# Performance work log

Hardware: AMD Instinct MI355X
Metric: run time of the kernel (lower is better)

The kernel has to match this reference:

```python
import jax, jax.numpy as jnp
from jax import lax
import numpy as np

B, L, D = 16, 512, 256
F, K = 256, 3
M = 2048
EPS = 1e-5


def setup_inputs() -> dict:
    key = jax.random.key(0)
    ks = jax.random.split(key, 12)
    x = jax.random.normal(ks[0], (B, L, D), jnp.float32)
    # integer durations >= 1, sum over L <= 3*512 = 1536 < M, as in training targets
    target = jax.random.randint(ks[1], (B, L), 1, 4)
    s = 0.02
    conv1_w = jax.random.normal(ks[2], (F, D, K), jnp.float32) * s
    conv1_b = jnp.zeros((F,), jnp.float32)
    ln1_g = jnp.ones((F,), jnp.float32)
    ln1_b = jnp.zeros((F,), jnp.float32)
    conv2_w = jax.random.normal(ks[3], (F, F, K), jnp.float32) * s
    conv2_b = jnp.zeros((F,), jnp.float32)
    ln2_g = jnp.ones((F,), jnp.float32)
    ln2_b = jnp.zeros((F,), jnp.float32)
    lin_w = jax.random.normal(ks[4], (F, 1), jnp.float32) * s
    lin_b = jnp.zeros((1,), jnp.float32)
    return dict(x=x, target=target, mel_max_length=M,
                conv1_w=conv1_w, conv1_b=conv1_b, ln1_g=ln1_g, ln1_b=ln1_b,
                conv2_w=conv2_w, conv2_b=conv2_b, ln2_g=ln2_g, ln2_b=ln2_b,
                lin_w=lin_w, lin_b=lin_b)


def _layer_norm(h, g, b):
    mu = jnp.mean(h, axis=-1, keepdims=True)
    var = jnp.mean(jnp.square(h - mu), axis=-1, keepdims=True)
    return (h - mu) * lax.rsqrt(var + EPS) * g + b


def _conv1d(h_bld, w, b):
    # h: (B, L, C_in), w: (C_out, C_in, K) -> (B, L, C_out), SAME padding
    pad = (w.shape[-1] - 1) // 2
    h = jnp.transpose(h_bld, (0, 2, 1))  # (B, C, L)
    h = lax.conv_general_dilated(h, w, (1,), [(pad, pad)],
                                 dimension_numbers=('NCH', 'OIH', 'NCH'))
    return jnp.transpose(h + b[None, :, None], (0, 2, 1))


def _duration_predictor(x, conv1_w, conv1_b, ln1_g, ln1_b,
                        conv2_w, conv2_b, ln2_g, ln2_b, lin_w, lin_b):
    # FastSpeech duration predictor (eval mode: dropout = identity)
    h = jax.nn.relu(_layer_norm(_conv1d(x, conv1_w, conv1_b), ln1_g, ln1_b))
    h = jax.nn.relu(_layer_norm(_conv1d(h, conv2_w, conv2_b), ln2_g, ln2_b))
    return jax.nn.relu(h @ lin_w + lin_b)[..., 0]  # (B, L)


def _length_regulate(x, dur, mel_max_length):
    # alignment[b,m,l] = 1 iff cs[l-1] <= m < cs[l]  (exactly the scatter+diff trick
    # of create_alignment, padded to mel_max_length as in the original F.pad)
    cs = jnp.cumsum(dur, axis=1)              # (B, L) inclusive cumsum
    prev = cs - dur                           # exclusive cumsum
    m = jnp.arange(mel_max_length)[None, :, None]  # (1, M, 1)
    align = ((m >= prev[:, None, :]) & (m < cs[:, None, :])).astype(x.dtype)  # (B,M,L)
    return jnp.einsum('bml,bld->bmd', align, x)


def reference(x, target, mel_max_length, conv1_w, conv1_b, ln1_g, ln1_b,
              conv2_w, conv2_b, ln2_g, ln2_b, lin_w, lin_b):
    dup = _duration_predictor(x, conv1_w, conv1_b, ln1_g, ln1_b,
                              conv2_w, conv2_b, ln2_g, ln2_b, lin_w, lin_b)
    output = _length_regulate(x, target, mel_max_length)
    return (output, dup)
```

## Files before the change

kernel.cpp:

```cpp
#include <hip/hip_runtime.h>
#include <hip/hip_bf16.h>

#define Bn 16
#define Ln 512
#define Cn 256
#define Fn 256
#define Kn 3
#define Mn 2048

#define NKSTEP 24
#define MT 32
#define XS_PS 264
#define NCONVBLK 256

typedef __attribute__((ext_vector_type(8))) short short8;
typedef __attribute__((ext_vector_type(4))) float f32x4;

static __device__ __forceinline__ unsigned short f2bf(float f) {
    unsigned int u = __float_as_uint(f);
    return (unsigned short)((u + 0x7fff + ((u >> 16) & 1)) >> 16);
}

__global__ __launch_bounds__(256) void pack_scan(
    const float* __restrict__ w1, const float* __restrict__ w2,
    unsigned short* __restrict__ bp1, unsigned short* __restrict__ bp2,
    const int* __restrict__ target, int* __restrict__ map)
{
    __shared__ int ss[256];
    const int blk = blockIdx.x;
    const int t = threadIdx.x;
    if (blk < 1536) {
        int i = blk * 256 + t;
        const float* w = w1;
        unsigned short* bp = bp1;
        if (i >= Fn * Cn * Kn) { i -= Fn * Cn * Kn; w = w2; bp = bp2; }
        int j    = i & 7;
        int lane = (i >> 3) & 63;
        int nt   = (i >> 9) & 15;
        int s    = i >> 13;
        int kap = s * 32 + ((lane >> 4) * 8) + j;
        int k = kap >> 8;
        int d = kap & 255;
        int f = nt * 16 + (lane & 15);
        bp[i] = f2bf(w[(f * Cn + d) * Kn + k]);
    } else {
        int b = blk - 1536;
        int v0 = target[b * Ln + 2 * t];
        int v1 = target[b * Ln + 2 * t + 1];
        ss[t] = v0 + v1;
        __syncthreads();
        for (int off = 1; off < 256; off <<= 1) {
            int add = (t >= off) ? ss[t - off] : 0;
            __syncthreads();
            ss[t] += add;
            __syncthreads();
        }
        int S     = ss[t];
        int total = ss[255];
        int cs1   = S;
        int cs0   = S - v1;
        int prev0 = cs0 - v0;
        for (int m = prev0; m < cs0; ++m) map[b * Mn + m] = 2 * t;
        for (int m = cs0;   m < cs1; ++m) map[b * Mn + m] = 2 * t + 1;
        for (int m = total + t; m < Mn; m += 256) map[b * Mn + m] = -1;
    }
}

template <bool IS_F32_IN, bool DO_LINEAR, bool WITH_REG>
__global__ __launch_bounds__(256) void conv_mfma(
    const void* __restrict__ in_,
    const unsigned short* __restrict__ bp,
    const float* __restrict__ bias,
    const float* __restrict__ gamma,
    const float* __restrict__ beta,
    const float* __restrict__ lw,
    const float* __restrict__ lb,
    unsigned short* __restrict__ hout,
    float* __restrict__ dup,
    const float* __restrict__ gx,
    const int* __restrict__ gmap,
    float* __restrict__ gout)
{
    __shared__ __align__(16) unsigned short xs[(MT + 2) * XS_PS];
    __shared__ float2 red[MT][4];
    __shared__ float  red2[MT][4];

    const int t = threadIdx.x;

    if (WITH_REG && blockIdx.x >= NCONVBLK) {
        int e4 = (blockIdx.x - NCONVBLK) * 256 + t;
        int d4 = e4 & 63;
        int bm = e4 >> 6;
        int b  = bm >> 11;
        int l  = gmap[bm];
        float4 val = make_float4(0.f, 0.f, 0.f, 0.f);
        if (l >= 0) val = *((const float4*)(gx + (size_t)(b * Ln + l) * Cn) + d4);
        ((float4*)gout)[e4] = val;
        return;
    }

    const int b  = blockIdx.x >> 4;
    const int l0 = (blockIdx.x & 15) * MT;

    if (IS_F32_IN) {
        const float* in = (const float*)in_;
        for (int idx = t; idx < (MT + 2) * 64; idx += 256) {
            int row = idx >> 6;
            int c4  = (idx & 63) * 4;
            int l = l0 + row - 1;
            float4 v = make_float4(0.f, 0.f, 0.f, 0.f);
            if (l >= 0 && l < Ln) v = *(const float4*)&in[((size_t)b * Ln + l) * Cn + c4];
            unsigned int lo = (unsigned int)f2bf(v.x) | ((unsigned int)f2bf(v.y) << 16);
            unsigned int hi = (unsigned int)f2bf(v.z) | ((unsigned int)f2bf(v.w) << 16);
            *(uint2*)&xs[row * XS_PS + c4] = make_uint2(lo, hi);
        }
    } else {
        const unsigned short* in = (const unsigned short*)in_;
        for (int idx = t; idx < (MT + 2) * 32; idx += 256) {
            int row = idx >> 5;
            int c8  = (idx & 31) * 8;
            int l = l0 + row - 1;
            uint4 v = make_uint4(0u, 0u, 0u, 0u);
            if (l >= 0 && l < Ln) v = *(const uint4*)&in[((size_t)b * Ln + l) * Cn + c8];
            *(uint4*)&xs[row * XS_PS + c8] = v;
        }
    }
    __syncthreads();

    const int lane = t & 63;
    const int wv   = t >> 6;
    const int mrow = lane & 15;
    const int q    = lane >> 4;

    f32x4  acc[2][4] = {};
    short8 bfr[2][4];
    short8 afr[2][2];

    auto loadB = [&](int s, int slot) {
        const unsigned short* p = bp + (size_t)((s * 16 + wv * 4) * 64 + lane) * 8;
        #pragma unroll
        for (int i = 0; i < 4; ++i)
            bfr[slot][i] = *(const short8*)(p + (size_t)i * 64 * 8);
    };
    auto loadA = [&](int s, int slot) {
        const int k    = s >> 3;
        const int dcol = (s & 7) * 32 + q * 8;
        #pragma unroll
        for (int mt = 0; mt < 2; ++mt)
            afr[slot][mt] = *(const short8*)&xs[(mt * 16 + mrow + k) * XS_PS + dcol];
    };

    loadB(0, 0); loadA(0, 0);
    loadB(1, 1); loadA(1, 1);

    #pragma unroll 2
    for (int s = 0; s < NKSTEP; ++s) {
        const int slot = s & 1;
        #pragma unroll
        for (int mt = 0; mt < 2; ++mt)
            #pragma unroll
            for (int i = 0; i < 4; ++i)
                acc[mt][i] = __builtin_amdgcn_mfma_f32_16x16x32_bf16(
                    afr[slot][mt], bfr[slot][i], acc[mt][i], 0, 0, 0);
        const int sn = (s + 2 < NKSTEP) ? (s + 2) : s;
        loadB(sn, slot);
        loadA(sn, slot);
    }

    float gv[4], bv[4], lwv[4], biasv[4];
    #pragma unroll
    for (int i = 0; i < 4; ++i) {
        int col = wv * 64 + i * 16 + mrow;
        biasv[i] = bias[col];
        gv[i]    = gamma[col];
        bv[i]    = beta[col];
        if (DO_LINEAR) lwv[i] = lw[col];
    }
    #pragma unroll
    for (int mt = 0; mt < 2; ++mt)
        #pragma unroll
        for (int i = 0; i < 4; ++i)
            #pragma unroll
            for (int r = 0; r < 4; ++r)
                acc[mt][i][r] += biasv[i];

    #pragma unroll
    for (int mt = 0; mt < 2; ++mt)
        #pragma unroll
        for (int r = 0; r < 4; ++r) {
            float s  = acc[mt][0][r] + acc[mt][1][r] + acc[mt][2][r] + acc[mt][3][r];
            float sq = acc[mt][0][r] * acc[mt][0][r] + acc[mt][1][r] * acc[mt][1][r]
                     + acc[mt][2][r] * acc[mt][2][r] + acc[mt][3][r] * acc[mt][3][r];
            #pragma unroll
            for (int off = 1; off <= 8; off <<= 1) {
                s  += __shfl_xor(s,  off, 64);
                sq += __shfl_xor(sq, off, 64);
            }
            if (mrow == 0) red[mt * 16 + q * 4 + r][wv] = make_float2(s, sq);
        }
    __syncthreads();

    float muv[2][4], rsv[2][4];
    #pragma unroll
    for (int mt = 0; mt < 2; ++mt)
        #pragma unroll
        for (int r = 0; r < 4; ++r) {
            int row = mt * 16 + q * 4 + r;
            float2 p0 = red[row][0], p1 = red[row][1], p2 = red[row][2], p3 = red[row][3];
            float s  = p0.x + p1.x + p2.x + p3.x;
            float sq = p0.y + p1.y + p2.y + p3.y;
            float mu  = s * (1.f / 256.f);
            float var = sq * (1.f / 256.f) - mu * mu;
            muv[mt][r] = mu;
            rsv[mt][r] = rsqrtf(var + 1e-5f);
        }

    if (!DO_LINEAR) {
        #pragma unroll
        for (int mt = 0; mt < 2; ++mt)
            #pragma unroll
            for (int r = 0; r < 4; ++r) {
                int l = l0 + mt * 16 + q * 4 + r;
                size_t base = ((size_t)b * Ln + l) * Fn;
                #pragma unroll
                for (int i = 0; i < 4; ++i) {
                    float o = fmaxf((acc[mt][i][r] - muv[mt][r]) * rsv[mt][r] * gv[i] + bv[i], 0.f);
                    hout[base + wv * 64 + i * 16 + mrow] = f2bf(o);
                }
            }
    } else {
        #pragma unroll
        for (int mt = 0; mt < 2; ++mt)
            #pragma unroll
            for (int r = 0; r < 4; ++r) {
                float dot = 0.f;
                #pragma unroll
                for (int i = 0; i < 4; ++i) {
                    float o = fmaxf((acc[mt][i][r] - muv[mt][r]) * rsv[mt][r] * gv[i] + bv[i], 0.f);
                    dot += o * lwv[i];
                }
                #pragma unroll
                for (int off = 1; off <= 8; off <<= 1)
                    dot += __shfl_xor(dot, off, 64);
                if (mrow == 0) red2[mt * 16 + q * 4 + r][wv] = dot;
            }
        __syncthreads();
        if (t < MT) {
            float d = red2[t][0] + red2[t][1] + red2[t][2] + red2[t][3];
            dup[b * Ln + l0 + t] = fmaxf(d + lb[0], 0.f);
        }
    }
}

extern "C" void kernel_launch(void* const* d_in, const int* in_sizes, int n_in,
                              void* d_out, int out_size, void* d_ws, size_t ws_size,
                              hipStream_t stream) {
    const float* x    = (const float*)d_in[0];
    const int*   targ = (const int*)d_in[1];
    const float* c1w = (const float*)d_in[3];
    const float* c1b = (const float*)d_in[4];
    const float* g1  = (const float*)d_in[5];
    const float* be1 = (const float*)d_in[6];
    const float* c2w = (const float*)d_in[7];
    const float* c2b = (const float*)d_in[8];
    const float* g2  = (const float*)d_in[9];
    const float* be2 = (const float*)d_in[10];
    const float* lw  = (const float*)d_in[11];
    const float* lb  = (const float*)d_in[12];

    float* out     = (float*)d_out;
    float* out_dup = out + (size_t)Bn * Mn * Cn;

    char* ws = (char*)d_ws;
    unsigned short* bp1 = (unsigned short*)ws;
    unsigned short* bp2 = (unsigned short*)(ws + 393216);
    unsigned short* h1  = (unsigned short*)(ws + 2 * 393216);
    int*            map = (int*)(ws + 2 * 393216 + 4194304);

    pack_scan<<<1552, 256, 0, stream>>>(c1w, c2w, bp1, bp2, targ, map);

    conv_mfma<true, false, true><<<NCONVBLK + (Bn * Mn * Cn / 4) / 256, 256, 0, stream>>>(
        (const void*)x, bp1, c1b, g1, be1, nullptr, nullptr, h1, nullptr,
        x, map, out);

    conv_mfma<false, true, false><<<NCONVBLK, 256, 0, stream>>>(
        (const void*)h1, bp2, c2b, g2, be2, lw, lb, nullptr, out_dup,
        nullptr, nullptr, nullptr);
}
```

Baseline: 116.6 us.

## Fuse pack, scan, both convs and gather into one cooperative kernel

```diff
diff --git a/kernel.cpp b/kernel.cpp
--- a/kernel.cpp
+++ b/kernel.cpp
@@ -1,5 +1,8 @@
 #include <hip/hip_runtime.h>
 #include <hip/hip_bf16.h>
+#include <hip/hip_cooperative_groups.h>
+
+namespace cg = cooperative_groups;
 
 #define Bn 16
 #define Ln 512
@@ -11,7 +14,6 @@
 #define NKSTEP 24
 #define MT 32
 #define XS_PS 264
-#define NCONVBLK 256
 
 typedef __attribute__((ext_vector_type(8))) short short8;
 typedef __attribute__((ext_vector_type(4))) float f32x4;
@@ -21,53 +23,21 @@
     return (unsigned short)((u + 0x7fff + ((u >> 16) & 1)) >> 16);
 }
 
-__global__ __launch_bounds__(256) void pack_scan(
-    const float* __restrict__ w1, const float* __restrict__ w2,
-    unsigned short* __restrict__ bp1, unsigned short* __restrict__ bp2,
-    const int* __restrict__ target, int* __restrict__ map)
+static __device__ __forceinline__ void gather_one(
+    const float* __restrict__ gx, const int* __restrict__ gmap,
+    float* __restrict__ gout, int e4)
 {
-    __shared__ int ss[256];
-    const int blk = blockIdx.x;
-    const int t = threadIdx.x;
-    if (blk < 1536) {
-        int i = blk * 256 + t;
-        const float* w = w1;
-        unsigned short* bp = bp1;
-        if (i >= Fn * Cn * Kn) { i -= Fn * Cn * Kn; w = w2; bp = bp2; }
-        int j    = i & 7;
-        int lane = (i >> 3) & 63;
-        int nt   = (i >> 9) & 15;
-        int s    = i >> 13;
-        int kap = s * 32 + ((lane >> 4) * 8) + j;
-        int k = kap >> 8;
-        int d = kap & 255;
-        int f = nt * 16 + (lane & 15);
-        bp[i] = f2bf(w[(f * Cn + d) * Kn + k]);
-    } else {
-        int b = blk - 1536;
-        int v0 = target[b * Ln + 2 * t];
-        int v1 = target[b * Ln + 2 * t + 1];
-        ss[t] = v0 + v1;
-        __syncthreads();
-        for (int off = 1; off < 256; off <<= 1) {
-            int add = (t >= off) ? ss[t - off] : 0;
-            __syncthreads();
-            ss[t] += add;
-            __syncthreads();
-        }
-        int S     = ss[t];
-        int total = ss[255];
-        int cs1   = S;
-        int cs0   = S - v1;
-        int prev0 = cs0 - v0;
-        for (int m = prev0; m < cs0; ++m) map[b * Mn + m] = 2 * t;
-        for (int m = cs0;   m < cs1; ++m) map[b * Mn + m] = 2 * t + 1;
-        for (int m = total + t; m < Mn; m += 256) map[b * Mn + m] = -1;
-    }
-}
-
-template <bool IS_F32_IN, bool DO_LINEAR, bool WITH_REG>
-__global__ __launch_bounds__(256) void conv_mfma(
+    int d4 = e4 & 63;
+    int bm = e4 >> 6;
+    int b  = bm >> 11;
+    int l  = gmap[bm];
+    float4 val = make_float4(0.f, 0.f, 0.f, 0.f);
+    if (l >= 0) val = *((const float4*)(gx + (size_t)(b * Ln + l) * Cn) + d4);
+    ((float4*)gout)[e4] = val;
+}
+
+template <bool IS_F32_IN, bool DO_LINEAR>
+static __device__ __forceinline__ void conv_phase(
     const void* __restrict__ in_,
     const unsigned short* __restrict__ bp,
     const float* __restrict__ bias,
@@ -77,30 +47,11 @@
     const float* __restrict__ lb,
     unsigned short* __restrict__ hout,
     float* __restrict__ dup,
-    const float* __restrict__ gx,
-    const int* __restrict__ gmap,
-    float* __restrict__ gout)
+    int cblk, int t,
+    unsigned short* xs, float2 (*red)[4], float (*red2)[4])
 {
-    __shared__ __align__(16) unsigned short xs[(MT + 2) * XS_PS];
-    __shared__ float2 red[MT][4];
-    __shared__ float  red2[MT][4];
-
-    const int t = threadIdx.x;
-
-    if (WITH_REG && blockIdx.x >= NCONVBLK) {
-        int e4 = (blockIdx.x - NCONVBLK) * 256 + t;
-        int d4 = e4 & 63;
-        int bm = e4 >> 6;
-        int b  = bm >> 11;
-        int l  = gmap[bm];
-        float4 val = make_float4(0.f, 0.f, 0.f, 0.f);
-        if (l >= 0) val = *((const float4*)(gx + (size_t)(b * Ln + l) * Cn) + d4);
-        ((float4*)gout)[e4] = val;
-        return;
-    }
-
-    const int b  = blockIdx.x >> 4;
-    const int l0 = (blockIdx.x & 15) * MT;
+    const int b  = cblk >> 4;
+    const int l0 = (cblk & 15) * MT;
 
     if (IS_F32_IN) {
         const float* in = (const float*)in_;
@@ -252,6 +203,78 @@
     }
 }
 
+__global__ __launch_bounds__(256) void fused(
+    const float* __restrict__ x, const int* __restrict__ target,
+    const float* __restrict__ c1w, const float* __restrict__ c1b,
+    const float* __restrict__ g1,  const float* __restrict__ be1,
+    const float* __restrict__ c2w, const float* __restrict__ c2b,
+    const float* __restrict__ g2,  const float* __restrict__ be2,
+    const float* __restrict__ lw,  const float* __restrict__ lb,
+    unsigned short* __restrict__ bp1, unsigned short* __restrict__ bp2,
+    unsigned short* __restrict__ h1,  int* __restrict__ map,
+    float* __restrict__ out, float* __restrict__ out_dup)
+{
+    __shared__ __align__(16) unsigned short xs[(MT + 2) * XS_PS];
+    __shared__ float2 red[MT][4];
+    __shared__ float  red2[MT][4];
+    __shared__ int    ss[256];
+
+    const int blk = blockIdx.x;
+    const int t   = threadIdx.x;
+    cg::grid_group grid = cg::this_grid();
+
+    if (blk < 16) {
+        const int bb = blk;
+        int v0 = target[bb * Ln + 2 * t];
+        int v1 = target[bb * Ln + 2 * t + 1];
+        ss[t] = v0 + v1;
+        __syncthreads();
+        for (int off = 1; off < 256; off <<= 1) {
+            int add = (t >= off) ? ss[t - off] : 0;
+            __syncthreads();
+            ss[t] += add;
+            __syncthreads();
+        }
+        int S     = ss[t];
+        int total = ss[255];
+        int cs1   = S;
+        int cs0   = S - v1;
+        int prev0 = cs0 - v0;
+        for (int m = prev0; m < cs0; ++m) map[bb * Mn + m] = 2 * t;
+        for (int m = cs0;   m < cs1; ++m) map[bb * Mn + m] = 2 * t + 1;
+        for (int m = total + t; m < Mn; m += 256) map[bb * Mn + m] = -1;
+    } else if (blk < 208) {
+        int v = (blk - 16) * 256 + t;
+        const float* w = c1w;
+        unsigned short* bp = bp1;
+        if (v >= 24576) { v -= 24576; w = c2w; bp = bp2; }
+        int lane = v & 63, nt = (v >> 6) & 15, s = v >> 10;
+        int f    = nt * 16 + (lane & 15);
+        int kap0 = s * 32 + (lane >> 4) * 8;
+        const float* p = w + ((size_t)f * Cn + (kap0 & 255)) * Kn + (kap0 >> 8);
+        short8 o;
+        #pragma unroll
+        for (int j = 0; j < 8; ++j) o[j] = (short)f2bf(p[3 * j]);
+        *(short8*)(bp + (size_t)v * 8) = o;
+    }
+
+    grid.sync();
+
+    conv_phase<true, false>(x, bp1, c1b, g1, be1, nullptr, nullptr, h1, nullptr,
+                            blk, t, xs, red, red2);
+    {
+        const int base = blk * 256 + t;
+        #pragma unroll 4
+        for (int i = 0; i < 32; ++i)
+            gather_one(x, map, out, base + i * 65536);
+    }
+
+    grid.sync();
+
+    conv_phase<false, true>(h1, bp2, c2b, g2, be2, lw, lb, nullptr, out_dup,
+                            blk, t, xs, red, red2);
+}
+
 extern "C" void kernel_launch(void* const* d_in, const int* in_sizes, int n_in,
                               void* d_out, int out_size, void* d_ws, size_t ws_size,
                               hipStream_t stream) {
@@ -277,13 +300,14 @@
     unsigned short* h1  = (unsigned short*)(ws + 2 * 393216);
     int*            map = (int*)(ws + 2 * 393216 + 4194304);
 
-    pack_scan<<<1552, 256, 0, stream>>>(c1w, c2w, bp1, bp2, targ, map);
-
-    conv_mfma<true, false, true><<<NCONVBLK + (Bn * Mn * Cn / 4) / 256, 256, 0, stream>>>(
-        (const void*)x, bp1, c1b, g1, be1, nullptr, nullptr, h1, nullptr,
-        x, map, out);
-
-    conv_mfma<false, true, false><<<NCONVBLK, 256, 0, stream>>>(
-        (const void*)h1, bp2, c2b, g2, be2, lw, lb, nullptr, out_dup,
-        nullptr, nullptr, nullptr);
-}
+    void* args[] = {
+        (void*)&x, (void*)&targ,
+        (void*)&c1w, (void*)&c1b, (void*)&g1, (void*)&be1,
+        (void*)&c2w, (void*)&c2b, (void*)&g2, (void*)&be2,
+        (void*)&lw, (void*)&lb,
+        (void*)&bp1, (void*)&bp2, (void*)&h1, (void*)&map,
+        (void*)&out, (void*)&out_dup
+    };
+    hipLaunchCooperativeKernel((const void*)fused, dim3(256), dim3(256),
+                               args, 0, stream);
+}
```

Measured after the change: 203.3 us. 1.74x slower.

## Fuse both conv layers into one kernel with halo recompute of layer one

Applied to the files above, without the earlier changes.

```diff
diff --git a/kernel.cpp b/kernel.cpp
--- a/kernel.cpp
+++ b/kernel.cpp
@@ -11,6 +11,9 @@
 #define NKSTEP 24
 #define MT 32
 #define XS_PS 264
+#define XROWS 50
+#define HROWS 48
+#define HOFF  8
 #define NCONVBLK 256
 
 typedef __attribute__((ext_vector_type(8))) short short8;
@@ -29,24 +32,10 @@
     __shared__ int ss[256];
     const int blk = blockIdx.x;
     const int t = threadIdx.x;
-    if (blk < 1536) {
-        int i = blk * 256 + t;
-        const float* w = w1;
-        unsigned short* bp = bp1;
-        if (i >= Fn * Cn * Kn) { i -= Fn * Cn * Kn; w = w2; bp = bp2; }
-        int j    = i & 7;
-        int lane = (i >> 3) & 63;
-        int nt   = (i >> 9) & 15;
-        int s    = i >> 13;
-        int kap = s * 32 + ((lane >> 4) * 8) + j;
-        int k = kap >> 8;
-        int d = kap & 255;
-        int f = nt * 16 + (lane & 15);
-        bp[i] = f2bf(w[(f * Cn + d) * Kn + k]);
-    } else {
-        int b = blk - 1536;
-        int v0 = target[b * Ln + 2 * t];
-        int v1 = target[b * Ln + 2 * t + 1];
+    if (blk < 16) {
+        const int bb = blk;
+        int v0 = target[bb * Ln + 2 * t];
+        int v1 = target[bb * Ln + 2 * t + 1];
         ss[t] = v0 + v1;
         __syncthreads();
         for (int off = 1; off < 256; off <<= 1) {
@@ -60,70 +49,66 @@
         int cs1   = S;
         int cs0   = S - v1;
         int prev0 = cs0 - v0;
-        for (int m = prev0; m < cs0; ++m) map[b * Mn + m] = 2 * t;
-        for (int m = cs0;   m < cs1; ++m) map[b * Mn + m] = 2 * t + 1;
-        for (int m = total + t; m < Mn; m += 256) map[b * Mn + m] = -1;
+        for (int m = prev0; m < cs0; ++m) map[bb * Mn + m] = 2 * t;
+        for (int m = cs0;   m < cs1; ++m) map[bb * Mn + m] = 2 * t + 1;
+        for (int m = total + t; m < Mn; m += 256) map[bb * Mn + m] = -1;
+    } else {
+        int v = (blk - 16) * 256 + t;
+        const float* w = w1;
+        unsigned short* bp = bp1;
+        if (v >= 24576) { v -= 24576; w = w2; bp = bp2; }
+        int lane = v & 63, nt = (v >> 6) & 15, s = v >> 10;
+        int f    = nt * 16 + (lane & 15);
+        int kap0 = s * 32 + (lane >> 4) * 8;
+        const float* p = w + ((size_t)f * Cn + (kap0 & 255)) * Kn + (kap0 >> 8);
+        short8 o;
+        #pragma unroll
+        for (int j = 0; j < 8; ++j) o[j] = (short)f2bf(p[3 * j]);
+        *(short8*)(bp + (size_t)v * 8) = o;
     }
 }
 
-template <bool IS_F32_IN, bool DO_LINEAR, bool WITH_REG>
-__global__ __launch_bounds__(256) void conv_mfma(
-    const void* __restrict__ in_,
-    const unsigned short* __restrict__ bp,
-    const float* __restrict__ bias,
-    const float* __restrict__ gamma,
-    const float* __restrict__ beta,
-    const float* __restrict__ lw,
-    const float* __restrict__ lb,
-    unsigned short* __restrict__ hout,
-    float* __restrict__ dup,
-    const float* __restrict__ gx,
+__global__ __launch_bounds__(256, 4) void conv12_gather(
+    const float* __restrict__ x,
+    const unsigned short* __restrict__ bp1,
+    const unsigned short* __restrict__ bp2,
+    const float* __restrict__ c1b, const float* __restrict__ g1, const float* __restrict__ be1,
+    const float* __restrict__ c2b, const float* __restrict__ g2, const float* __restrict__ be2,
+    const float* __restrict__ lw,  const float* __restrict__ lb,
     const int* __restrict__ gmap,
-    float* __restrict__ gout)
+    float* __restrict__ out,
+    float* __restrict__ dup)
 {
-    __shared__ __align__(16) unsigned short xs[(MT + 2) * XS_PS];
-    __shared__ float2 red[MT][4];
+    __shared__ __align__(16) unsigned short xs[XROWS * XS_PS];
+    __shared__ float2 red[HROWS][4];
     __shared__ float  red2[MT][4];
 
     const int t = threadIdx.x;
 
-    if (WITH_REG && blockIdx.x >= NCONVBLK) {
+    if (blockIdx.x >= NCONVBLK) {
         int e4 = (blockIdx.x - NCONVBLK) * 256 + t;
         int d4 = e4 & 63;
         int bm = e4 >> 6;
         int b  = bm >> 11;
         int l  = gmap[bm];
         float4 val = make_float4(0.f, 0.f, 0.f, 0.f);
-        if (l >= 0) val = *((const float4*)(gx + (size_t)(b * Ln + l) * Cn) + d4);
-        ((float4*)gout)[e4] = val;
+        if (l >= 0) val = *((const float4*)(x + (size_t)(b * Ln + l) * Cn) + d4);
+        ((float4*)out)[e4] = val;
         return;
     }
 
     const int b  = blockIdx.x >> 4;
     const int l0 = (blockIdx.x & 15) * MT;
 
-    if (IS_F32_IN) {
-        const float* in = (const float*)in_;
-        for (int idx = t; idx < (MT + 2) * 64; idx += 256) {
-            int row = idx >> 6;
-            int c4  = (idx & 63) * 4;
-            int l = l0 + row - 1;
-            float4 v = make_float4(0.f, 0.f, 0.f, 0.f);
-            if (l >= 0 && l < Ln) v = *(const float4*)&in[((size_t)b * Ln + l) * Cn + c4];
-            unsigned int lo = (unsigned int)f2bf(v.x) | ((unsigned int)f2bf(v.y) << 16);
-            unsigned int hi = (unsigned int)f2bf(v.z) | ((unsigned int)f2bf(v.w) << 16);
-            *(uint2*)&xs[row * XS_PS + c4] = make_uint2(lo, hi);
-        }
-    } else {
-        const unsigned short* in = (const unsigned short*)in_;
-        for (int idx = t; idx < (MT + 2) * 32; idx += 256) {
-            int row = idx >> 5;
-            int c8  = (idx & 31) * 8;
-            int l = l0 + row - 1;
-            uint4 v = make_uint4(0u, 0u, 0u, 0u);
-            if (l >= 0 && l < Ln) v = *(const uint4*)&in[((size_t)b * Ln + l) * Cn + c8];
-            *(uint4*)&xs[row * XS_PS + c8] = v;
-        }
+    for (int idx = t; idx < XROWS * 64; idx += 256) {
+        int row = idx >> 6;
+        int c4  = (idx & 63) * 4;
+        int l = l0 - 9 + row;
+        float4 v = make_float4(0.f, 0.f, 0.f, 0.f);
+        if (l >= 0 && l < Ln) v = *(const float4*)&x[((size_t)b * Ln + l) * Cn + c4];
+        unsigned int lo = (unsigned int)f2bf(v.x) | ((unsigned int)f2bf(v.y) << 16);
+        unsigned int hi = (unsigned int)f2bf(v.z) | ((unsigned int)f2bf(v.w) << 16);
+        *(uint2*)&xs[row * XS_PS + c4] = make_uint2(lo, hi);
     }
     __syncthreads();
 
@@ -132,111 +117,197 @@
     const int mrow = lane & 15;
     const int q    = lane >> 4;
 
-    f32x4  acc[2][4] = {};
+    f32x4  acc1[3][4] = {};
     short8 bfr[2][4];
-    short8 afr[2][2];
-
-    auto loadB = [&](int s, int slot) {
-        const unsigned short* p = bp + (size_t)((s * 16 + wv * 4) * 64 + lane) * 8;
+    short8 afr[2][3];
+
+    auto loadB1 = [&](int s, int slot) {
+        const unsigned short* p = bp1 + (size_t)((s * 16 + wv * 4) * 64 + lane) * 8;
         #pragma unroll
         for (int i = 0; i < 4; ++i)
             bfr[slot][i] = *(const short8*)(p + (size_t)i * 64 * 8);
     };
-    auto loadA = [&](int s, int slot) {
+    auto loadA1 = [&](int s, int slot) {
         const int k    = s >> 3;
         const int dcol = (s & 7) * 32 + q * 8;
         #pragma unroll
-        for (int mt = 0; mt < 2; ++mt)
+        for (int mt = 0; mt < 3; ++mt)
             afr[slot][mt] = *(const short8*)&xs[(mt * 16 + mrow + k) * XS_PS + dcol];
     };
 
-    loadB(0, 0); loadA(0, 0);
-    loadB(1, 1); loadA(1, 1);
+    loadB1(0, 0); loadA1(0, 0);
+    loadB1(1, 1); loadA1(1, 1);
 
     #pragma unroll 2
     for (int s = 0; s < NKSTEP; ++s) {
         const int slot = s & 1;
         #pragma unroll
-        for (int mt = 0; mt < 2; ++mt)
+        for (int mt = 0; mt < 3; ++mt)
             #pragma unroll
             for (int i = 0; i < 4; ++i)
-                acc[mt][i] = __builtin_amdgcn_mfma_f32_16x16x32_bf16(
-                    afr[slot][mt], bfr[slot][i], acc[mt][i], 0, 0, 0);
+                acc1[mt][i] = __builtin_amdgcn_mfma_f32_16x16x32_bf16(
+                    afr[slot][mt], bfr[slot][i], acc1[mt][i], 0, 0, 0);
         const int sn = (s + 2 < NKSTEP) ? (s + 2) : s;
-        loadB(sn, slot);
-        loadA(sn, slot);
-    }
-
-    float gv[4], bv[4], lwv[4], biasv[4];
-    #pragma unroll
-    for (int i = 0; i < 4; ++i) {
-        int col = wv * 64 + i * 16 + mrow;
-        biasv[i] = bias[col];
-        gv[i]    = gamma[col];
-        bv[i]    = beta[col];
-        if (DO_LINEAR) lwv[i] = lw[col];
-    }
-    #pragma unroll
-    for (int mt = 0; mt < 2; ++mt)
+        loadB1(sn, slot);
+        loadA1(sn, slot);
+    }
+
+    {
+        float gv[4], bv[4], biasv[4];
+        #pragma unroll
+        for (int i = 0; i < 4; ++i) {
+            int col = wv * 64 + i * 16 + mrow;
+            biasv[i] = c1b[col];
+            gv[i]    = g1[col];
+            bv[i]    = be1[col];
+        }
+        #pragma unroll
+        for (int mt = 0; mt < 3; ++mt)
+            #pragma unroll
+            for (int i = 0; i < 4; ++i)
+                #pragma unroll
+                for (int r = 0; r < 4; ++r)
+                    acc1[mt][i][r] += biasv[i];
+
+        #pragma unroll
+        for (int mt = 0; mt < 3; ++mt)
+            #pragma unroll
+            for (int r = 0; r < 4; ++r) {
+                float s  = acc1[mt][0][r] + acc1[mt][1][r] + acc1[mt][2][r] + acc1[mt][3][r];
+                float sq = acc1[mt][0][r] * acc1[mt][0][r] + acc1[mt][1][r] * acc1[mt][1][r]
+                         + acc1[mt][2][r] * acc1[mt][2][r] + acc1[mt][3][r] * acc1[mt][3][r];
+                #pragma unroll
+                for (int off = 1; off <= 8; off <<= 1) {
+                    s  += __shfl_xor(s,  off, 64);
+                    sq += __shfl_xor(sq, off, 64);
+                }
+                if (mrow == 0) red[mt * 16 + q * 4 + r][wv] = make_float2(s, sq);
+            }
+        __syncthreads();
+
+        float muv[3][4], rsv[3][4];
+        #pragma unroll
+        for (int mt = 0; mt < 3; ++mt)
+            #pragma unroll
+            for (int r = 0; r < 4; ++r) {
+                int row = mt * 16 + q * 4 + r;
+                float2 p0 = red[row][0], p1 = red[row][1], p2 = red[row][2], p3 = red[row][3];
+                float s  = p0.x + p1.x + p2.x + p3.x;
+                float sq = p0.y + p1.y + p2.y + p3.y;
+                float mu  = s * (1.f / 256.f);
+                float var = sq * (1.f / 256.f) - mu * mu;
+                muv[mt][r] = mu;
+                rsv[mt][r] = rsqrtf(var + 1e-5f);
+            }
+
+        #pragma unroll
+        for (int mt = 0; mt < 3; ++mt)
+            #pragma unroll
+            for (int r = 0; r < 4; ++r) {
+                int jr = mt * 16 + q * 4 + r;
+                int l  = l0 - HOFF + jr;
+                bool ok = (l >= 0 && l < Ln);
+                #pragma unroll
+                for (int i = 0; i < 4; ++i) {
+                    float o = ok ? fmaxf((acc1[mt][i][r] - muv[mt][r]) * rsv[mt][r] * gv[i] + bv[i], 0.f)
+                                 : 0.f;
+                    xs[jr * XS_PS + (wv * 64 + i * 16 + mrow)] = f2bf(o);
+                }
+            }
+    }
+    __syncthreads();
+
+    f32x4  acc2[2][4] = {};
+    short8 afr2[2][2];
+
+    auto loadB2 = [&](int s, int slot) {
+        const unsigned short* p = bp2 + (size_t)((s * 16 + wv * 4) * 64 + lane) * 8;
         #pragma unroll
         for (int i = 0; i < 4; ++i)
-            #pragma unroll
-            for (int r = 0; r < 4; ++r)
-                acc[mt][i][r] += biasv[i];
-
-    #pragma unroll
-    for (int mt = 0; mt < 2; ++mt)
-        #pragma unroll
-        for (int r = 0; r < 4; ++r) {
-            float s  = acc[mt][0][r] + acc[mt][1][r] + acc[mt][2][r] + acc[mt][3][r];
-            float sq = acc[mt][0][r] * acc[mt][0][r] + acc[mt][1][r] * acc[mt][1][r]
-                     + acc[mt][2][r] * acc[mt][2][r] + acc[mt][3][r] * acc[mt][3][r];
-            #pragma unroll
-            for (int off = 1; off <= 8; off <<= 1) {
-                s  += __shfl_xor(s,  off, 64);
-                sq += __shfl_xor(sq, off, 64);
-            }
-            if (mrow == 0) red[mt * 16 + q * 4 + r][wv] = make_float2(s, sq);
+            bfr[slot][i] = *(const short8*)(p + (size_t)i * 64 * 8);
+    };
+    auto loadA2 = [&](int s, int slot) {
+        const int k    = s >> 3;
+        const int dcol = (s & 7) * 32 + q * 8;
+        #pragma unroll
+        for (int mt = 0; mt < 2; ++mt)
+            afr2[slot][mt] = *(const short8*)&xs[(mt * 16 + mrow + k + 7) * XS_PS + dcol];
+    };
+
+    loadB2(0, 0); loadA2(0, 0);
+    loadB2(1, 1); loadA2(1, 1);
+
+    #pragma unroll 2
+    for (int s = 0; s < NKSTEP; ++s) {
+        const int slot = s & 1;
+        #pragma unroll
+        for (int mt = 0; mt < 2; ++mt)
+            #pragma unroll
+            for (int i = 0; i < 4; ++i)
+                acc2[mt][i] = __builtin_amdgcn_mfma_f32_16x16x32_bf16(
+                    afr2[slot][mt], bfr[slot][i], acc2[mt][i], 0, 0, 0);
+        const int sn = (s + 2 < NKSTEP) ? (s + 2) : s;
+        loadB2(sn, slot);
+        loadA2(sn, slot);
+    }
+
+    {
+        float gv[4], bv[4], biasv[4], lwv[4];
+        #pragma unroll
+        for (int i = 0; i < 4; ++i) {
+            int col = wv * 64 + i * 16 + mrow;
+            biasv[i] = c2b[col];
+            gv[i]    = g2[col];
+            bv[i]    = be2[col];
+            lwv[i]   = lw[col];
         }
-    __syncthreads();
-
-    float muv[2][4], rsv[2][4];
-    #pragma unroll
-    for (int mt = 0; mt < 2; ++mt)
-        #pragma unroll
-        for (int r = 0; r < 4; ++r) {
-            int row = mt * 16 + q * 4 + r;
-            float2 p0 = red[row][0], p1 = red[row][1], p2 = red[row][2], p3 = red[row][3];
-            float s  = p0.x + p1.x + p2.x + p3.x;
-            float sq = p0.y + p1.y + p2.y + p3.y;
-            float mu  = s * (1.f / 256.f);
-            float var = sq * (1.f / 256.f) - mu * mu;
-            muv[mt][r] = mu;
-            rsv[mt][r] = rsqrtf(var + 1e-5f);
-        }
-
-    if (!DO_LINEAR) {
-        #pragma unroll
-        for (int mt = 0; mt < 2; ++mt)
-            #pragma unroll
-            for (int r = 0; r < 4; ++r) {
-                int l = l0 + mt * 16 + q * 4 + r;
-                size_t base = ((size_t)b * Ln + l) * Fn;
+        #pragma unroll
+        for (int mt = 0; mt < 2; ++mt)
+            #pragma unroll
+            for (int i = 0; i < 4; ++i)
+                #pragma unroll
+                for (int r = 0; r < 4; ++r)
+                    acc2[mt][i][r] += biasv[i];
+
+        #pragma unroll
+        for (int mt = 0; mt < 2; ++mt)
+            #pragma unroll
+            for (int r = 0; r < 4; ++r) {
+                float s  = acc2[mt][0][r] + acc2[mt][1][r] + acc2[mt][2][r] + acc2[mt][3][r];
+                float sq = acc2[mt][0][r] * acc2[mt][0][r] + acc2[mt][1][r] * acc2[mt][1][r]
+                         + acc2[mt][2][r] * acc2[mt][2][r] + acc2[mt][3][r] * acc2[mt][3][r];
+                #pragma unroll
+                for (int off = 1; off <= 8; off <<= 1) {
+                    s  += __shfl_xor(s,  off, 64);
+                    sq += __shfl_xor(sq, off, 64);
+                }
+                if (mrow == 0) red[mt * 16 + q * 4 + r][wv] = make_float2(s, sq);
+            }
+        __syncthreads();
+
+        float muv[2][4], rsv[2][4];
+        #pragma unroll
+        for (int mt = 0; mt < 2; ++mt)
+            #pragma unroll
+            for (int r = 0; r < 4; ++r) {
+                int row = mt * 16 + q * 4 + r;
+                float2 p0 = red[row][0], p1 = red[row][1], p2 = red[row][2], p3 = red[row][3];
+                float s  = p0.x + p1.x + p2.x + p3.x;
+                float sq = p0.y + p1.y + p2.y + p3.y;
+                float mu  = s * (1.f / 256.f);
+                float var = sq * (1.f / 256.f) - mu * mu;
+                muv[mt][r] = mu;
+                rsv[mt][r] = rsqrtf(var + 1e-5f);
+            }
+
+        #pragma unroll
+        for (int mt = 0; mt < 2; ++mt)
+            #pragma unroll
+            for (int r = 0; r < 4; ++r) {
+                float dot = 0.f;
                 #pragma unroll
                 for (int i = 0; i < 4; ++i) {
-                    float o = fmaxf((acc[mt][i][r] - muv[mt][r]) * rsv[mt][r] * gv[i] + bv[i], 0.f);
-                    hout[base + wv * 64 + i * 16 + mrow] = f2bf(o);
-                }
-            }
-    } else {
-        #pragma unroll
-        for (int mt = 0; mt < 2; ++mt)
-            #pragma unroll
-            for (int r = 0; r < 4; ++r) {
-                float dot = 0.f;
-                #pragma unroll
-                for (int i = 0; i < 4; ++i) {
-                    float o = fmaxf((acc[mt][i][r] - muv[mt][r]) * rsv[mt][r] * gv[i] + bv[i], 0.f);
+                    float o = fmaxf((acc2[mt][i][r] - muv[mt][r]) * rsv[mt][r] * gv[i] + bv[i], 0.f);
                     dot += o * lwv[i];
                 }
                 #pragma unroll
@@ -274,16 +345,11 @@
     char* ws = (char*)d_ws;
     unsigned short* bp1 = (unsigned short*)ws;
     unsigned short* bp2 = (unsigned short*)(ws + 393216);
-    unsigned short* h1  = (unsigned short*)(ws + 2 * 393216);
-    int*            map = (int*)(ws + 2 * 393216 + 4194304);
-
-    pack_scan<<<1552, 256, 0, stream>>>(c1w, c2w, bp1, bp2, targ, map);
-
-    conv_mfma<true, false, true><<<NCONVBLK + (Bn * Mn * Cn / 4) / 256, 256, 0, stream>>>(
-        (const void*)x, bp1, c1b, g1, be1, nullptr, nullptr, h1, nullptr,
-        x, map, out);
-
-    conv_mfma<false, true, false><<<NCONVBLK, 256, 0, stream>>>(
-        (const void*)h1, bp2, c2b, g2, be2, lw, lb, nullptr, out_dup,
-        nullptr, nullptr, nullptr);
+    int*            map = (int*)(ws + 2 * 393216);
+
+    pack_scan<<<208, 256, 0, stream>>>(c1w, c2w, bp1, bp2, targ, map);
+
+    conv12_gather<<<NCONVBLK + (Bn * Mn * Cn / 4) / 256, 256, 0, stream>>>(
+        x, bp1, bp2, c1b, g1, be1, c2b, g2, be2, lw, lb,
+        map, out, out_dup);
 }
```

Result: slower. 132.7 us (+13.8%).

## Split length-regulate gather across both conv kernels and vectorize weight packing

Applied to the files above, without the earlier changes.

```diff
diff --git a/kernel.cpp b/kernel.cpp
--- a/kernel.cpp
+++ b/kernel.cpp
@@ -12,6 +12,7 @@
 #define MT 32
 #define XS_PS 264
 #define NCONVBLK 256
+#define NGHALF 1024
 
 typedef __attribute__((ext_vector_type(8))) short short8;
 typedef __attribute__((ext_vector_type(4))) float f32x4;
@@ -29,24 +30,10 @@
     __shared__ int ss[256];
     const int blk = blockIdx.x;
     const int t = threadIdx.x;
-    if (blk < 1536) {
-        int i = blk * 256 + t;
-        const float* w = w1;
-        unsigned short* bp = bp1;
-        if (i >= Fn * Cn * Kn) { i -= Fn * Cn * Kn; w = w2; bp = bp2; }
-        int j    = i & 7;
-        int lane = (i >> 3) & 63;
-        int nt   = (i >> 9) & 15;
-        int s    = i >> 13;
-        int kap = s * 32 + ((lane >> 4) * 8) + j;
-        int k = kap >> 8;
-        int d = kap & 255;
-        int f = nt * 16 + (lane & 15);
-        bp[i] = f2bf(w[(f * Cn + d) * Kn + k]);
-    } else {
-        int b = blk - 1536;
-        int v0 = target[b * Ln + 2 * t];
-        int v1 = target[b * Ln + 2 * t + 1];
+    if (blk < 16) {
+        const int bb = blk;
+        int v0 = target[bb * Ln + 2 * t];
+        int v1 = target[bb * Ln + 2 * t + 1];
         ss[t] = v0 + v1;
         __syncthreads();
         for (int off = 1; off < 256; off <<= 1) {
@@ -60,13 +47,26 @@
         int cs1   = S;
         int cs0   = S - v1;
         int prev0 = cs0 - v0;
-        for (int m = prev0; m < cs0; ++m) map[b * Mn + m] = 2 * t;
-        for (int m = cs0;   m < cs1; ++m) map[b * Mn + m] = 2 * t + 1;
-        for (int m = total + t; m < Mn; m += 256) map[b * Mn + m] = -1;
-    }
-}
-
-template <bool IS_F32_IN, bool DO_LINEAR, bool WITH_REG>
+        for (int m = prev0; m < cs0; ++m) map[bb * Mn + m] = 2 * t;
+        for (int m = cs0;   m < cs1; ++m) map[bb * Mn + m] = 2 * t + 1;
+        for (int m = total + t; m < Mn; m += 256) map[bb * Mn + m] = -1;
+    } else {
+        int v = (blk - 16) * 256 + t;
+        const float* w = w1;
+        unsigned short* bp = bp1;
+        if (v >= 24576) { v -= 24576; w = w2; bp = bp2; }
+        int lane = v & 63, nt = (v >> 6) & 15, s = v >> 10;
+        int f    = nt * 16 + (lane & 15);
+        int kap0 = s * 32 + (lane >> 4) * 8;
+        const float* p = w + ((size_t)f * Cn + (kap0 & 255)) * Kn + (kap0 >> 8);
+        short8 o;
+        #pragma unroll
+        for (int j = 0; j < 8; ++j) o[j] = (short)f2bf(p[3 * j]);
+        *(short8*)(bp + (size_t)v * 8) = o;
+    }
+}
+
+template <bool IS_F32_IN, bool DO_LINEAR, int E4OFF>
 __global__ __launch_bounds__(256) void conv_mfma(
     const void* __restrict__ in_,
     const unsigned short* __restrict__ bp,
@@ -87,15 +87,25 @@
 
     const int t = threadIdx.x;
 
-    if (WITH_REG && blockIdx.x >= NCONVBLK) {
-        int e4 = (blockIdx.x - NCONVBLK) * 256 + t;
-        int d4 = e4 & 63;
-        int bm = e4 >> 6;
-        int b  = bm >> 11;
-        int l  = gmap[bm];
-        float4 val = make_float4(0.f, 0.f, 0.f, 0.f);
-        if (l >= 0) val = *((const float4*)(gx + (size_t)(b * Ln + l) * Cn) + d4);
-        ((float4*)gout)[e4] = val;
+    if (blockIdx.x >= NCONVBLK) {
+        const int base = (blockIdx.x - NCONVBLK) * 256 + t;
+        int lv[4];
+        #pragma unroll
+        for (int i = 0; i < 4; ++i)
+            lv[i] = gmap[(E4OFF + base + i * 262144) >> 6];
+        float4 val[4];
+        #pragma unroll
+        for (int i = 0; i < 4; ++i) {
+            int e4 = E4OFF + base + i * 262144;
+            int d4 = e4 & 63;
+            int b  = e4 >> 17;
+            val[i] = make_float4(0.f, 0.f, 0.f, 0.f);
+            if (lv[i] >= 0)
+                val[i] = *((const float4*)(gx + (size_t)(b * Ln + lv[i]) * Cn) + d4);
+        }
+        #pragma unroll
+        for (int i = 0; i < 4; ++i)
+            ((float4*)gout)[E4OFF + base + i * 262144] = val[i];
         return;
     }
 
@@ -277,13 +287,13 @@
     unsigned short* h1  = (unsigned short*)(ws + 2 * 393216);
     int*            map = (int*)(ws + 2 * 393216 + 4194304);
 
-    pack_scan<<<1552, 256, 0, stream>>>(c1w, c2w, bp1, bp2, targ, map);
-
-    conv_mfma<true, false, true><<<NCONVBLK + (Bn * Mn * Cn / 4) / 256, 256, 0, stream>>>(
+    pack_scan<<<208, 256, 0, stream>>>(c1w, c2w, bp1, bp2, targ, map);
+
+    conv_mfma<true, false, 0><<<NCONVBLK + NGHALF, 256, 0, stream>>>(
         (const void*)x, bp1, c1b, g1, be1, nullptr, nullptr, h1, nullptr,
         x, map, out);
 
-    conv_mfma<false, true, false><<<NCONVBLK, 256, 0, stream>>>(
+    conv_mfma<false, true, 1048576><<<NCONVBLK + NGHALF, 256, 0, stream>>>(
         (const void*)h1, bp2, c2b, g2, be2, lw, lb, nullptr, out_dup,
-        nullptr, nullptr, nullptr);
-}
+        x, map, out);
+}
```

After: 116.8 us. Within noise of the previous version (+0.2%).
